# Kernel optimization log

Hardware: AMD Instinct MI355X
Metric: run time of the kernel (lower is better)

The kernel has to match this reference:

```python
import jax, jax.numpy as jnp
import numpy as np

N = 50000      # nodes
E = 800000     # edges (before self-loops)
IN = 128       # in_channels
H = 4          # heads
F = 32         # out_channels per head
NEG_SLOPE = 0.2  # GATConv default negative_slope


def setup_inputs() -> dict:
    key = jax.random.key(0)
    k1, k2, k3, k4, k5 = jax.random.split(key, 5)
    x = jax.random.normal(k1, (N, IN), dtype=jnp.float32)
    edge_index = jax.random.randint(k2, (2, E), 0, N, dtype=jnp.int32)
    W = jax.random.normal(k3, (IN, H * F), dtype=jnp.float32) * 0.05
    att_src = jax.random.normal(k4, (H, F), dtype=jnp.float32) * 0.05
    att_dst = jax.random.normal(k5, (H, F), dtype=jnp.float32) * 0.05
    bias = jnp.zeros((H * F,), dtype=jnp.float32)
    return {"x": x, "edge_index": edge_index, "W": W,
            "att_src": att_src, "att_dst": att_dst, "bias": bias}


def reference(x, edge_index, W, att_src, att_dst, bias):
    n = x.shape[0]
    # Linear projection, split into heads: [N, H, F]
    xp = (x @ W).reshape(n, H, F)
    # add_self_loops=True (GATConv default)
    loop = jnp.arange(n, dtype=edge_index.dtype)
    src = jnp.concatenate([edge_index[0], loop])  # [E+N]
    dst = jnp.concatenate([edge_index[1], loop])  # [E+N]
    # Per-node attention logits: [N, H]
    a_s = jnp.einsum('nhf,hf->nh', xp, att_src)
    a_d = jnp.einsum('nhf,hf->nh', xp, att_dst)
    # Edge logits + LeakyReLU: [E+N, H]
    e = jax.nn.leaky_relu(a_s[src] + a_d[dst], NEG_SLOPE)
    # Segment softmax over incoming edges of each dst node
    m = jax.ops.segment_max(e, dst, num_segments=n)  # every node has a self-loop
    e = jnp.exp(e - m[dst])
    denom = jax.ops.segment_sum(e, dst, num_segments=n)
    alpha = e / denom[dst]                     # [E+N, H]
    # Weighted aggregation of source features: [N, H, F]
    msg = alpha[:, :, None] * xp[src]
    out = jax.ops.segment_sum(msg, dst, num_segments=n)
    out = out.reshape(n, H * F) + bias         # concat heads + bias
    return jax.nn.relu(out)                    # wrapper activation (dropout = eval identity)
```

## Files before the change

### kernel.cpp

```cpp
#include <hip/hip_runtime.h>

#define HEADS 4
#define BSHIFT 8

typedef __attribute__((ext_vector_type(8))) short bf16x8;
typedef __attribute__((ext_vector_type(4))) float f32x4;

__device__ __forceinline__ unsigned short f2bf(float f) {
  unsigned u = __builtin_bit_cast(unsigned, f);
  u = (u + 0x7FFFu + ((u >> 16) & 1u)) >> 16;
  return (unsigned short)u;
}
__device__ __forceinline__ float bf2f(unsigned short s) {
  return __builtin_bit_cast(float, (unsigned)s << 16);
}
__device__ __forceinline__ float bf_lo(unsigned u) {
  return __builtin_bit_cast(float, u << 16);
}
__device__ __forceinline__ float bf_hi(unsigned u) {
  return __builtin_bit_cast(float, u & 0xFFFF0000u);
}

__global__ __launch_bounds__(256) void k_gemm(
    const float* __restrict__ x, const float* __restrict__ W,
    const float* __restrict__ att_src, const float* __restrict__ att_dst,
    unsigned* __restrict__ xpb, float* __restrict__ a_s, float* __restrict__ a_d,
    int* __restrict__ ghist, int n)
{
  __shared__ unsigned short xb[64 * 136];
  __shared__ unsigned short Wt[128 * 136];
  const int tid = threadIdx.x;
  const int row0 = blockIdx.x * 64;
  if (blockIdx.x == 0) ghist[tid] = 0;

  for (int u = tid; u < 2048; u += 256) {
    const int r = u >> 5, cq = u & 31;
    float4 v = make_float4(0.f, 0.f, 0.f, 0.f);
    if (row0 + r < n) v = ((const float4*)x)[(size_t)(row0 + r) * 32 + cq];
    unsigned short* p = &xb[r * 136 + cq * 4];
    p[0] = f2bf(v.x); p[1] = f2bf(v.y); p[2] = f2bf(v.z); p[3] = f2bf(v.w);
  }
  for (int u = tid; u < 4096; u += 256) {
    const int k = u >> 5, cq = u & 31;
    const float4 v = ((const float4*)W)[u];
    Wt[(4 * cq + 0) * 136 + k] = f2bf(v.x);
    Wt[(4 * cq + 1) * 136 + k] = f2bf(v.y);
    Wt[(4 * cq + 2) * 136 + k] = f2bf(v.z);
    Wt[(4 * cq + 3) * 136 + k] = f2bf(v.w);
  }
  __syncthreads();

  const int wv = tid >> 6;
  const int lane = tid & 63;
  const int r = lane & 15, g = lane >> 4;

  f32x4 acc[8];
#pragma unroll
  for (int t = 0; t < 8; ++t) acc[t] = (f32x4){0.f, 0.f, 0.f, 0.f};

  bf16x8 afr[4];
#pragma unroll
  for (int kc = 0; kc < 4; ++kc)
    afr[kc] = *(const bf16x8*)&xb[(16 * wv + r) * 136 + kc * 32 + g * 8];

#pragma unroll
  for (int kc = 0; kc < 4; ++kc) {
#pragma unroll
    for (int t = 0; t < 8; ++t) {
      const bf16x8 bfr = *(const bf16x8*)&Wt[(16 * t + r) * 136 + kc * 32 + g * 8];
      acc[t] = __builtin_amdgcn_mfma_f32_16x16x32_bf16(afr[kc], bfr, acc[t], 0, 0, 0);
    }
  }
  __syncthreads();

  unsigned short* obuf = Wt;
#pragma unroll
  for (int t = 0; t < 8; ++t) {
#pragma unroll
    for (int j = 0; j < 4; ++j)
      obuf[(16 * wv + 4 * g + j) * 132 + 16 * t + r] = f2bf(acc[t][j]);
  }
  __syncthreads();

  {
    const int row = tid >> 2, h = tid & 3;
    float ps = 0.f, pd = 0.f;
    const unsigned short* orow = &obuf[row * 132 + 32 * h];
#pragma unroll 8
    for (int j = 0; j < 32; ++j) {
      const float v = bf2f(orow[j]);
      ps += v * att_src[32 * h + j];
      pd += v * att_dst[32 * h + j];
    }
    if (row0 + row < n) {
      a_s[(row0 + row) * HEADS + h] = ps;
      a_d[(row0 + row) * HEADS + h] = pd;
    }
  }
  for (int u = tid; u < 2048; u += 256) {
    const int row = u >> 5, q = u & 31;
    if (row0 + row < n)
      ((uint2*)xpb)[(size_t)(row0 + row) * 32 + q] = *(const uint2*)&obuf[row * 132 + q * 4];
  }
}

__global__ __launch_bounds__(256) void k_hist(
    const int* __restrict__ dst, int* __restrict__ ghist, int E)
{
  __shared__ int h[256];
  const int t = threadIdx.x;
  h[t] = 0;
  __syncthreads();
  int i = blockIdx.x * 1024 + t;
#pragma unroll
  for (int k = 0; k < 4; ++k, i += 256)
    if (i < E) atomicAdd(&h[dst[i] >> BSHIFT], 1);
  __syncthreads();
  if (h[t]) atomicAdd(&ghist[t], h[t]);
}

__global__ __launch_bounds__(256) void k_bscan(
    const int* __restrict__ ghist, int* __restrict__ gstart, int* __restrict__ gcur)
{
  __shared__ int wsum[4];
  const int t = threadIdx.x, lane = t & 63, w = t >> 6;
  const int v = ghist[t];
  int s = v;
#pragma unroll
  for (int o = 1; o < 64; o <<= 1) { int u = __shfl_up(s, o); if (lane >= o) s += u; }
  if (lane == 63) wsum[w] = s;
  __syncthreads();
  int add = 0;
  for (int k = 0; k < w; ++k) add += wsum[k];
  const int excl = add + s - v;
  gstart[t] = excl;
  gcur[t] = excl;
  if (t == 255) gstart[256] = excl + v;
}

__global__ __launch_bounds__(256) void k_part(
    const int* __restrict__ src, const int* __restrict__ dst,
    int* __restrict__ gcur, unsigned* __restrict__ pbuf, int E)
{
  __shared__ unsigned sortbuf[4096];
  __shared__ int hist[256], lstart[256], lcur[256], wbase[256];
  __shared__ int wsum[4];
  const int t = threadIdx.x;
  const int e0 = blockIdx.x * 4096;
  const int cnt = min(4096, E - e0);
  hist[t] = 0;
  __syncthreads();
  for (int i = t; i < cnt; i += 256)
    atomicAdd(&hist[dst[e0 + i] >> BSHIFT], 1);
  __syncthreads();
  const int lane = t & 63, w = t >> 6;
  const int v = hist[t];
  int s = v;
#pragma unroll
  for (int o = 1; o < 64; o <<= 1) { int u = __shfl_up(s, o); if (lane >= o) s += u; }
  if (lane == 63) wsum[w] = s;
  __syncthreads();
  int add = 0;
  for (int k = 0; k < w; ++k) add += wsum[k];
  const int ls = add + s - v;
  lstart[t] = ls;
  lcur[t] = ls;
  wbase[t] = (v > 0) ? atomicAdd(&gcur[t], v) : 0;
  __syncthreads();
  for (int i = t; i < cnt; i += 256) {
    const int d = dst[e0 + i], sE = src[e0 + i];
    const int r = atomicAdd(&lcur[d >> BSHIFT], 1);
    sortbuf[r] = ((unsigned)d << 16) | (unsigned)sE;
  }
  __syncthreads();
  for (int i = t; i < cnt; i += 256) {
    const unsigned p = sortbuf[i];
    const int b = (int)(p >> (16 + BSHIFT));
    pbuf[wbase[b] + (i - lstart[b])] = p;
  }
}

__global__ __launch_bounds__(256) void k_fill2(
    const unsigned* __restrict__ pbuf, const int* __restrict__ gstart,
    int* __restrict__ offs, int* __restrict__ eidx, int n, int E)
{
  __shared__ int cnt[256], base[256];
  __shared__ int wsum[4];
  const int b = blockIdx.x, t = threadIdx.x;
  const int node0 = b << BSHIFT;
  const int ebeg = gstart[b], eend = gstart[b + 1];
  cnt[t] = 0;
  __syncthreads();
  for (int i = ebeg + t; i < eend; i += 256)
    atomicAdd(&cnt[(pbuf[i] >> 16) & 255], 1);
  __syncthreads();
  const int lane = t & 63, w = t >> 6;
  const int v = cnt[t];
  int s = v;
#pragma unroll
  for (int o = 1; o < 64; o <<= 1) { int u = __shfl_up(s, o); if (lane >= o) s += u; }
  if (lane == 63) wsum[w] = s;
  __syncthreads();
  int add = 0;
  for (int k = 0; k < w; ++k) add += wsum[k];
  base[t] = ebeg + add + s - v;
  if (node0 + t < n) offs[node0 + t] = base[t];
  __syncthreads();
  for (int i = ebeg + t; i < eend; i += 256) {
    const unsigned p = pbuf[i];
    const int pos = atomicAdd(&base[(p >> 16) & 255], 1);
    eidx[pos] = (int)(p & 0xFFFFu);
  }
  if (b == 0 && t == 0) offs[n] = E;
}

__global__ __launch_bounds__(256) void k_aggr(
    const unsigned* __restrict__ xpb, const float* __restrict__ a_s,
    const float* __restrict__ a_d, const int* __restrict__ offs,
    const int* __restrict__ eidx, const float* __restrict__ bias,
    float* __restrict__ out, int n)
{
  const int wid = (blockIdx.x * blockDim.x + threadIdx.x) >> 6;
  const int lane = threadIdx.x & 63;
  if (wid >= n) return;
  const int h = lane >> 4;

  const float adh = a_d[wid * HEADS + h];

  float l = a_s[wid * HEADS + h] + adh;
  l = l > 0.f ? l : 0.2f * l;
  const float pself = __expf(l);
  float den = pself;
  const unsigned uself = xpb[(size_t)wid * 64 + lane];
  float accx = pself * bf_lo(uself), accy = pself * bf_hi(uself);

  const int beg = offs[wid], end = offs[wid + 1];
  int e = beg;
  int nb = (end - beg) >> 2;

#define LOADB(s0, s1, s2, s3, u0, u1, u2, u3, b0, b1, b2, b3)            \
  {                                                                      \
    s0 = eidx[e]; s1 = eidx[e + 1]; s2 = eidx[e + 2]; s3 = eidx[e + 3];  \
    u0 = xpb[(size_t)s0 * 64 + lane]; b0 = a_s[s0 * HEADS + h];          \
    u1 = xpb[(size_t)s1 * 64 + lane]; b1 = a_s[s1 * HEADS + h];          \
    u2 = xpb[(size_t)s2 * 64 + lane]; b2 = a_s[s2 * HEADS + h];          \
    u3 = xpb[(size_t)s3 * 64 + lane]; b3 = a_s[s3 * HEADS + h];          \
    e += 4;                                                              \
  }
#define CONSUME(u0, u1, u2, u3, b0, b1, b2, b3)                          \
  {                                                                      \
    float l0 = b0 + adh; l0 = l0 > 0.f ? l0 : 0.2f * l0;                 \
    float l1 = b1 + adh; l1 = l1 > 0.f ? l1 : 0.2f * l1;                 \
    float l2 = b2 + adh; l2 = l2 > 0.f ? l2 : 0.2f * l2;                 \
    float l3 = b3 + adh; l3 = l3 > 0.f ? l3 : 0.2f * l3;                 \
    const float p0 = __expf(l0), p1 = __expf(l1);                        \
    const float p2 = __expf(l2), p3 = __expf(l3);                        \
    den += p0 + p1 + p2 + p3;                                            \
    accx += p0 * bf_lo(u0) + p1 * bf_lo(u1) + p2 * bf_lo(u2) + p3 * bf_lo(u3); \
    accy += p0 * bf_hi(u0) + p1 * bf_hi(u1) + p2 * bf_hi(u2) + p3 * bf_hi(u3); \
  }

  if (nb > 0) {
    int sa0, sa1, sa2, sa3, sb0, sb1, sb2, sb3;
    unsigned ua0, ua1, ua2, ua3, ub0, ub1, ub2, ub3;
    float ba0, ba1, ba2, ba3, bb0, bb1, bb2, bb3;
    LOADB(sa0, sa1, sa2, sa3, ua0, ua1, ua2, ua3, ba0, ba1, ba2, ba3);
    --nb;
    while (nb >= 2) {
      LOADB(sb0, sb1, sb2, sb3, ub0, ub1, ub2, ub3, bb0, bb1, bb2, bb3);
      CONSUME(ua0, ua1, ua2, ua3, ba0, ba1, ba2, ba3);
      LOADB(sa0, sa1, sa2, sa3, ua0, ua1, ua2, ua3, ba0, ba1, ba2, ba3);
      CONSUME(ub0, ub1, ub2, ub3, bb0, bb1, bb2, bb3);
      nb -= 2;
    }
    if (nb == 1) {
      LOADB(sb0, sb1, sb2, sb3, ub0, ub1, ub2, ub3, bb0, bb1, bb2, bb3);
      CONSUME(ua0, ua1, ua2, ua3, ba0, ba1, ba2, ba3);
      CONSUME(ub0, ub1, ub2, ub3, bb0, bb1, bb2, bb3);
    } else {
      CONSUME(ua0, ua1, ua2, ua3, ba0, ba1, ba2, ba3);
    }
  }
  for (; e < end; ++e) {
    const int s = eidx[e];
    const unsigned u = xpb[(size_t)s * 64 + lane];
    float lv = a_s[s * HEADS + h] + adh;
    lv = lv > 0.f ? lv : 0.2f * lv;
    const float p = __expf(lv);
    den += p;
    accx += p * bf_lo(u);
    accy += p * bf_hi(u);
  }
#undef LOADB
#undef CONSUME

  const float2 b2 = ((const float2*)bias)[lane];
  const float inv = 1.f / den;
  float ox = accx * inv + b2.x;
  float oy = accy * inv + b2.y;
  float2 o = make_float2(ox > 0.f ? ox : 0.f, oy > 0.f ? oy : 0.f);
  ((float2*)out)[(size_t)wid * 64 + lane] = o;
}

extern "C" void kernel_launch(void* const* d_in, const int* in_sizes, int n_in,
                              void* d_out, int out_size, void* d_ws, size_t ws_size,
                              hipStream_t stream) {
  const float* x       = (const float*)d_in[0];
  const int*   ei      = (const int*)d_in[1];
  const float* W       = (const float*)d_in[2];
  const float* att_src = (const float*)d_in[3];
  const float* att_dst = (const float*)d_in[4];
  const float* bias    = (const float*)d_in[5];
  float* out = (float*)d_out;
  const int n = in_sizes[0] / 128;
  const int E = in_sizes[1] / 2;
  const int* srce = ei;
  const int* dste = ei + E;

  char* ws = (char*)d_ws;
  size_t o = 0;
  unsigned* xpb = (unsigned*)(ws + o); o += (size_t)n * 128 * 2;
  o = (o + 255) & ~(size_t)255;
  float* a_s = (float*)(ws + o); o += (size_t)n * HEADS * 4;
  float* a_d = (float*)(ws + o); o += (size_t)n * HEADS * 4;
  int* ghist  = (int*)(ws + o);  o += 256 * 4;
  int* gstart = (int*)(ws + o);  o += 260 * 4;
  int* gcur   = (int*)(ws + o);  o += 256 * 4;
  int* offs   = (int*)(ws + o);  o += (size_t)(n + 4) * 4;
  int* eidx   = (int*)(ws + o);  o += (size_t)E * 4;
  unsigned* pbuf = (unsigned*)(ws + o); o += (size_t)E * 4;

  const int NB = (n + 255) >> BSHIFT;
  k_gemm<<<(n + 63) / 64, 256, 0, stream>>>(x, W, att_src, att_dst, xpb, a_s, a_d, ghist, n);
  k_hist<<<(E + 1023) / 1024, 256, 0, stream>>>(dste, ghist, E);
  k_bscan<<<1, 256, 0, stream>>>(ghist, gstart, gcur);
  k_part<<<(E + 4095) / 4096, 256, 0, stream>>>(srce, dste, gcur, pbuf, E);
  k_fill2<<<NB, 256, 0, stream>>>(pbuf, gstart, offs, eidx, n, E);
  k_aggr<<<(n + 3) / 4, 256, 0, stream>>>(xpb, a_s, a_d, offs, eidx, bias, out, n);
}
```

Measured before the change: 121.4 us.

## Precompute per-edge attention exponentials in CSR fill and pre-transpose W to bf16

The per-edge LeakyReLU and exp are moved out of the aggregation kernel into the CSR fill kernel, which writes a float4 of four per-head exponentials per edge in sorted order. The aggregation then reads those values instead of gathering a_s per source and computing exp once per lane. Separately, a small kernel converts and transposes W to bf16 once, so each GEMM block does vectorized copies instead of strided scalar conversions. This adds a 16-byte-per-edge buffer written and read back, plus an extra launch, in exchange for less repeated math and fewer scattered loads.

```diff
diff --git a/kernel.cpp b/kernel.cpp
--- a/kernel.cpp
+++ b/kernel.cpp
@@ -21,8 +21,16 @@
   return __builtin_bit_cast(float, u & 0xFFFF0000u);
 }
 
+__global__ __launch_bounds__(256) void k_wprep(
+    const float* __restrict__ W, unsigned short* __restrict__ Wtb)
+{
+  const int i = blockIdx.x * 256 + threadIdx.x;
+  const int c = i >> 7, k = i & 127;
+  Wtb[i] = f2bf(W[k * 128 + c]);
+}
+
 __global__ __launch_bounds__(256) void k_gemm(
-    const float* __restrict__ x, const float* __restrict__ W,
+    const float* __restrict__ x, const unsigned short* __restrict__ Wtb,
     const float* __restrict__ att_src, const float* __restrict__ att_dst,
     unsigned* __restrict__ xpb, float* __restrict__ a_s, float* __restrict__ a_d,
     int* __restrict__ ghist, int n)
@@ -40,13 +48,9 @@
     unsigned short* p = &xb[r * 136 + cq * 4];
     p[0] = f2bf(v.x); p[1] = f2bf(v.y); p[2] = f2bf(v.z); p[3] = f2bf(v.w);
   }
-  for (int u = tid; u < 4096; u += 256) {
-    const int k = u >> 5, cq = u & 31;
-    const float4 v = ((const float4*)W)[u];
-    Wt[(4 * cq + 0) * 136 + k] = f2bf(v.x);
-    Wt[(4 * cq + 1) * 136 + k] = f2bf(v.y);
-    Wt[(4 * cq + 2) * 136 + k] = f2bf(v.z);
-    Wt[(4 * cq + 3) * 136 + k] = f2bf(v.w);
+  for (int u = tid; u < 2048; u += 256) {
+    const int c = u >> 4, q = u & 15;
+    *(uint4*)&Wt[c * 136 + q * 8] = ((const uint4*)Wtb)[u];
   }
   __syncthreads();
 
@@ -182,14 +186,18 @@
 
 __global__ __launch_bounds__(256) void k_fill2(
     const unsigned* __restrict__ pbuf, const int* __restrict__ gstart,
-    int* __restrict__ offs, int* __restrict__ eidx, int n, int E)
+    const float* __restrict__ a_s, const float* __restrict__ a_d,
+    int* __restrict__ offs, int* __restrict__ eidx, float4* __restrict__ pflt,
+    int n, int E)
 {
   __shared__ int cnt[256], base[256];
+  __shared__ float4 adl[256];
   __shared__ int wsum[4];
   const int b = blockIdx.x, t = threadIdx.x;
   const int node0 = b << BSHIFT;
   const int ebeg = gstart[b], eend = gstart[b + 1];
   cnt[t] = 0;
+  if (node0 + t < n) adl[t] = ((const float4*)a_d)[node0 + t];
   __syncthreads();
   for (int i = ebeg + t; i < eend; i += 256)
     atomicAdd(&cnt[(pbuf[i] >> 16) & 255], 1);
@@ -208,8 +216,19 @@
   __syncthreads();
   for (int i = ebeg + t; i < eend; i += 256) {
     const unsigned p = pbuf[i];
-    const int pos = atomicAdd(&base[(p >> 16) & 255], 1);
-    eidx[pos] = (int)(p & 0xFFFFu);
+    const int dl = (p >> 16) & 255;
+    const int sn = (int)(p & 0xFFFFu);
+    const int pos = atomicAdd(&base[dl], 1);
+    eidx[pos] = sn;
+    const float4 as = ((const float4*)a_s)[sn];
+    const float4 ad = adl[dl];
+    float4 pv;
+    float l;
+    l = as.x + ad.x; l = fmaxf(l, 0.2f * l); pv.x = __expf(l);
+    l = as.y + ad.y; l = fmaxf(l, 0.2f * l); pv.y = __expf(l);
+    l = as.z + ad.z; l = fmaxf(l, 0.2f * l); pv.z = __expf(l);
+    l = as.w + ad.w; l = fmaxf(l, 0.2f * l); pv.w = __expf(l);
+    pflt[pos] = pv;
   }
   if (b == 0 && t == 0) offs[n] = E;
 }
@@ -217,18 +236,16 @@
 __global__ __launch_bounds__(256) void k_aggr(
     const unsigned* __restrict__ xpb, const float* __restrict__ a_s,
     const float* __restrict__ a_d, const int* __restrict__ offs,
-    const int* __restrict__ eidx, const float* __restrict__ bias,
-    float* __restrict__ out, int n)
+    const int* __restrict__ eidx, const float* __restrict__ pflt,
+    const float* __restrict__ bias, float* __restrict__ out, int n)
 {
   const int wid = (blockIdx.x * blockDim.x + threadIdx.x) >> 6;
   const int lane = threadIdx.x & 63;
   if (wid >= n) return;
   const int h = lane >> 4;
 
-  const float adh = a_d[wid * HEADS + h];
-
-  float l = a_s[wid * HEADS + h] + adh;
-  l = l > 0.f ? l : 0.2f * l;
+  float l = a_s[wid * HEADS + h] + a_d[wid * HEADS + h];
+  l = fmaxf(l, 0.2f * l);
   const float pself = __expf(l);
   float den = pself;
   const unsigned uself = xpb[(size_t)wid * 64 + lane];
@@ -238,23 +255,17 @@
   int e = beg;
   int nb = (end - beg) >> 2;
 
-#define LOADB(s0, s1, s2, s3, u0, u1, u2, u3, b0, b1, b2, b3)            \
+#define LOADB(s0, s1, s2, s3, u0, u1, u2, u3, p0, p1, p2, p3)            \
   {                                                                      \
     s0 = eidx[e]; s1 = eidx[e + 1]; s2 = eidx[e + 2]; s3 = eidx[e + 3];  \
-    u0 = xpb[(size_t)s0 * 64 + lane]; b0 = a_s[s0 * HEADS + h];          \
-    u1 = xpb[(size_t)s1 * 64 + lane]; b1 = a_s[s1 * HEADS + h];          \
-    u2 = xpb[(size_t)s2 * 64 + lane]; b2 = a_s[s2 * HEADS + h];          \
-    u3 = xpb[(size_t)s3 * 64 + lane]; b3 = a_s[s3 * HEADS + h];          \
+    p0 = pflt[(size_t)e * 4 + h];       u0 = xpb[(size_t)s0 * 64 + lane];\
+    p1 = pflt[(size_t)(e + 1) * 4 + h]; u1 = xpb[(size_t)s1 * 64 + lane];\
+    p2 = pflt[(size_t)(e + 2) * 4 + h]; u2 = xpb[(size_t)s2 * 64 + lane];\
+    p3 = pflt[(size_t)(e + 3) * 4 + h]; u3 = xpb[(size_t)s3 * 64 + lane];\
     e += 4;                                                              \
   }
-#define CONSUME(u0, u1, u2, u3, b0, b1, b2, b3)                          \
+#define CONSUME(u0, u1, u2, u3, p0, p1, p2, p3)                          \
   {                                                                      \
-    float l0 = b0 + adh; l0 = l0 > 0.f ? l0 : 0.2f * l0;                 \
-    float l1 = b1 + adh; l1 = l1 > 0.f ? l1 : 0.2f * l1;                 \
-    float l2 = b2 + adh; l2 = l2 > 0.f ? l2 : 0.2f * l2;                 \
-    float l3 = b3 + adh; l3 = l3 > 0.f ? l3 : 0.2f * l3;                 \
-    const float p0 = __expf(l0), p1 = __expf(l1);                        \
-    const float p2 = __expf(l2), p3 = __expf(l3);                        \
     den += p0 + p1 + p2 + p3;                                            \
     accx += p0 * bf_lo(u0) + p1 * bf_lo(u1) + p2 * bf_lo(u2) + p3 * bf_lo(u3); \
     accy += p0 * bf_hi(u0) + p1 * bf_hi(u1) + p2 * bf_hi(u2) + p3 * bf_hi(u3); \
@@ -263,30 +274,28 @@
   if (nb > 0) {
     int sa0, sa1, sa2, sa3, sb0, sb1, sb2, sb3;
     unsigned ua0, ua1, ua2, ua3, ub0, ub1, ub2, ub3;
-    float ba0, ba1, ba2, ba3, bb0, bb1, bb2, bb3;
-    LOADB(sa0, sa1, sa2, sa3, ua0, ua1, ua2, ua3, ba0, ba1, ba2, ba3);
+    float pa0, pa1, pa2, pa3, pb0, pb1, pb2, pb3;
+    LOADB(sa0, sa1, sa2, sa3, ua0, ua1, ua2, ua3, pa0, pa1, pa2, pa3);
     --nb;
     while (nb >= 2) {
-      LOADB(sb0, sb1, sb2, sb3, ub0, ub1, ub2, ub3, bb0, bb1, bb2, bb3);
-      CONSUME(ua0, ua1, ua2, ua3, ba0, ba1, ba2, ba3);
-      LOADB(sa0, sa1, sa2, sa3, ua0, ua1, ua2, ua3, ba0, ba1, ba2, ba3);
-      CONSUME(ub0, ub1, ub2, ub3, bb0, bb1, bb2, bb3);
+      LOADB(sb0, sb1, sb2, sb3, ub0, ub1, ub2, ub3, pb0, pb1, pb2, pb3);
+      CONSUME(ua0, ua1, ua2, ua3, pa0, pa1, pa2, pa3);
+      LOADB(sa0, sa1, sa2, sa3, ua0, ua1, ua2, ua3, pa0, pa1, pa2, pa3);
+      CONSUME(ub0, ub1, ub2, ub3, pb0, pb1, pb2, pb3);
       nb -= 2;
     }
     if (nb == 1) {
-      LOADB(sb0, sb1, sb2, sb3, ub0, ub1, ub2, ub3, bb0, bb1, bb2, bb3);
-      CONSUME(ua0, ua1, ua2, ua3, ba0, ba1, ba2, ba3);
-      CONSUME(ub0, ub1, ub2, ub3, bb0, bb1, bb2, bb3);
+      LOADB(sb0, sb1, sb2, sb3, ub0, ub1, ub2, ub3, pb0, pb1, pb2, pb3);
+      CONSUME(ua0, ua1, ua2, ua3, pa0, pa1, pa2, pa3);
+      CONSUME(ub0, ub1, ub2, ub3, pb0, pb1, pb2, pb3);
     } else {
-      CONSUME(ua0, ua1, ua2, ua3, ba0, ba1, ba2, ba3);
+      CONSUME(ua0, ua1, ua2, ua3, pa0, pa1, pa2, pa3);
     }
   }
   for (; e < end; ++e) {
     const int s = eidx[e];
     const unsigned u = xpb[(size_t)s * 64 + lane];
-    float lv = a_s[s * HEADS + h] + adh;
-    lv = lv > 0.f ? lv : 0.2f * lv;
-    const float p = __expf(lv);
+    const float p = pflt[(size_t)e * 4 + h];
     den += p;
     accx += p * bf_lo(u);
     accy += p * bf_hi(u);
@@ -323,18 +332,22 @@
   o = (o + 255) & ~(size_t)255;
   float* a_s = (float*)(ws + o); o += (size_t)n * HEADS * 4;
   float* a_d = (float*)(ws + o); o += (size_t)n * HEADS * 4;
+  unsigned short* Wtb = (unsigned short*)(ws + o); o += 128 * 128 * 2;
   int* ghist  = (int*)(ws + o);  o += 256 * 4;
   int* gstart = (int*)(ws + o);  o += 260 * 4;
   int* gcur   = (int*)(ws + o);  o += 256 * 4;
   int* offs   = (int*)(ws + o);  o += (size_t)(n + 4) * 4;
   int* eidx   = (int*)(ws + o);  o += (size_t)E * 4;
   unsigned* pbuf = (unsigned*)(ws + o); o += (size_t)E * 4;
+  o = (o + 15) & ~(size_t)15;
+  float4* pflt = (float4*)(ws + o); o += (size_t)E * 16;
 
   const int NB = (n + 255) >> BSHIFT;
-  k_gemm<<<(n + 63) / 64, 256, 0, stream>>>(x, W, att_src, att_dst, xpb, a_s, a_d, ghist, n);
+  k_wprep<<<64, 256, 0, stream>>>(W, Wtb);
+  k_gemm<<<(n + 63) / 64, 256, 0, stream>>>(x, Wtb, att_src, att_dst, xpb, a_s, a_d, ghist, n);
   k_hist<<<(E + 1023) / 1024, 256, 0, stream>>>(dste, ghist, E);
   k_bscan<<<1, 256, 0, stream>>>(ghist, gstart, gcur);
   k_part<<<(E + 4095) / 4096, 256, 0, stream>>>(srce, dste, gcur, pbuf, E);
-  k_fill2<<<NB, 256, 0, stream>>>(pbuf, gstart, offs, eidx, n, E);
-  k_aggr<<<(n + 3) / 4, 256, 0, stream>>>(xpb, a_s, a_d, offs, eidx, bias, out, n);
-}
+  k_fill2<<<NB, 256, 0, stream>>>(pbuf, gstart, a_s, a_d, offs, eidx, pflt, n, E);
+  k_aggr<<<(n + 3) / 4, 256, 0, stream>>>(xpb, a_s, a_d, offs, eidx, (const float*)pflt, bias, out, n);
+}
```

Result: slower. 125.1 us (+3.0%).

## Fuse GEMM, histogram and bucket scan into one launch with pre-transposed bf16 W

Applied to the files above, without the earlier changes.

Moves the W transpose and bf16 conversion into a small prep kernel so each GEMM block does one vectorized copy instead of a strided scatter into shared memory. The destination histogram and the bucket scan are merged into the GEMM launch as extra blocks, and the last histogram block, found through an atomic done counter, runs the scan. This drops two kernel launches and lets the histogram overlap the GEMM, at the cost of an extra small launch and a threadfence and atomic handshake. LeakyReLU is also rewritten as fmaxf in the aggregation kernel.

```diff
diff --git a/kernel.cpp b/kernel.cpp
--- a/kernel.cpp
+++ b/kernel.cpp
@@ -21,17 +21,65 @@
   return __builtin_bit_cast(float, u & 0xFFFF0000u);
 }
 
-__global__ __launch_bounds__(256) void k_gemm(
-    const float* __restrict__ x, const float* __restrict__ W,
+__global__ __launch_bounds__(256) void k_wprep(
+    const float* __restrict__ W, unsigned short* __restrict__ Wtb,
+    int* __restrict__ ghist, int* __restrict__ done)
+{
+  const int i = blockIdx.x * 256 + threadIdx.x;
+  const int c = i >> 7, k = i & 127;
+  Wtb[i] = f2bf(W[k * 128 + c]);
+  if (blockIdx.x == 0) {
+    ghist[threadIdx.x] = 0;
+    if (threadIdx.x == 0) *done = 0;
+  }
+}
+
+__global__ __launch_bounds__(256) void k_mega(
+    const float* __restrict__ x, const unsigned short* __restrict__ Wtb,
     const float* __restrict__ att_src, const float* __restrict__ att_dst,
     unsigned* __restrict__ xpb, float* __restrict__ a_s, float* __restrict__ a_d,
-    int* __restrict__ ghist, int n)
+    const int* __restrict__ dste, int* __restrict__ ghist, int* __restrict__ gstart,
+    int* __restrict__ gcur, int* __restrict__ done,
+    int n, int E, int GB, int NHB)
 {
   __shared__ unsigned short xb[64 * 136];
   __shared__ unsigned short Wt[128 * 136];
   const int tid = threadIdx.x;
+
+  if (blockIdx.x >= GB) {
+    int* h = (int*)xb;
+    h[tid] = 0;
+    __syncthreads();
+    int i = (blockIdx.x - GB) * 4096 + tid;
+#pragma unroll
+    for (int k = 0; k < 16; ++k, i += 256)
+      if (i < E) atomicAdd(&h[dste[i] >> BSHIFT], 1);
+    __syncthreads();
+    if (h[tid]) atomicAdd(&ghist[tid], h[tid]);
+    __threadfence();
+    __shared__ int lastFlag;
+    if (tid == 0) lastFlag = (atomicAdd(done, 1) == NHB - 1) ? 1 : 0;
+    __syncthreads();
+    if (lastFlag) {
+      __shared__ int wsum[4];
+      const int lane = tid & 63, w = tid >> 6;
+      const int v = atomicAdd(&ghist[tid], 0);
+      int s = v;
+#pragma unroll
+      for (int o = 1; o < 64; o <<= 1) { int u = __shfl_up(s, o); if (lane >= o) s += u; }
+      if (lane == 63) wsum[w] = s;
+      __syncthreads();
+      int add = 0;
+      for (int k = 0; k < w; ++k) add += wsum[k];
+      const int excl = add + s - v;
+      gstart[tid] = excl;
+      gcur[tid] = excl;
+      if (tid == 255) gstart[256] = excl + v;
+    }
+    return;
+  }
+
   const int row0 = blockIdx.x * 64;
-  if (blockIdx.x == 0) ghist[tid] = 0;
 
   for (int u = tid; u < 2048; u += 256) {
     const int r = u >> 5, cq = u & 31;
@@ -40,13 +88,9 @@
     unsigned short* p = &xb[r * 136 + cq * 4];
     p[0] = f2bf(v.x); p[1] = f2bf(v.y); p[2] = f2bf(v.z); p[3] = f2bf(v.w);
   }
-  for (int u = tid; u < 4096; u += 256) {
-    const int k = u >> 5, cq = u & 31;
-    const float4 v = ((const float4*)W)[u];
-    Wt[(4 * cq + 0) * 136 + k] = f2bf(v.x);
-    Wt[(4 * cq + 1) * 136 + k] = f2bf(v.y);
-    Wt[(4 * cq + 2) * 136 + k] = f2bf(v.z);
-    Wt[(4 * cq + 3) * 136 + k] = f2bf(v.w);
+  for (int u = tid; u < 2048; u += 256) {
+    const int c = u >> 4, q = u & 15;
+    *(uint4*)&Wt[c * 136 + q * 8] = ((const uint4*)Wtb)[u];
   }
   __syncthreads();
 
@@ -104,40 +148,6 @@
   }
 }
 
-__global__ __launch_bounds__(256) void k_hist(
-    const int* __restrict__ dst, int* __restrict__ ghist, int E)
-{
-  __shared__ int h[256];
-  const int t = threadIdx.x;
-  h[t] = 0;
-  __syncthreads();
-  int i = blockIdx.x * 1024 + t;
-#pragma unroll
-  for (int k = 0; k < 4; ++k, i += 256)
-    if (i < E) atomicAdd(&h[dst[i] >> BSHIFT], 1);
-  __syncthreads();
-  if (h[t]) atomicAdd(&ghist[t], h[t]);
-}
-
-__global__ __launch_bounds__(256) void k_bscan(
-    const int* __restrict__ ghist, int* __restrict__ gstart, int* __restrict__ gcur)
-{
-  __shared__ int wsum[4];
-  const int t = threadIdx.x, lane = t & 63, w = t >> 6;
-  const int v = ghist[t];
-  int s = v;
-#pragma unroll
-  for (int o = 1; o < 64; o <<= 1) { int u = __shfl_up(s, o); if (lane >= o) s += u; }
-  if (lane == 63) wsum[w] = s;
-  __syncthreads();
-  int add = 0;
-  for (int k = 0; k < w; ++k) add += wsum[k];
-  const int excl = add + s - v;
-  gstart[t] = excl;
-  gcur[t] = excl;
-  if (t == 255) gstart[256] = excl + v;
-}
-
 __global__ __launch_bounds__(256) void k_part(
     const int* __restrict__ src, const int* __restrict__ dst,
     int* __restrict__ gcur, unsigned* __restrict__ pbuf, int E)
@@ -228,7 +238,7 @@
   const float adh = a_d[wid * HEADS + h];
 
   float l = a_s[wid * HEADS + h] + adh;
-  l = l > 0.f ? l : 0.2f * l;
+  l = fmaxf(l, 0.2f * l);
   const float pself = __expf(l);
   float den = pself;
   const unsigned uself = xpb[(size_t)wid * 64 + lane];
@@ -249,10 +259,10 @@
   }
 #define CONSUME(u0, u1, u2, u3, b0, b1, b2, b3)                          \
   {                                                                      \
-    float l0 = b0 + adh; l0 = l0 > 0.f ? l0 : 0.2f * l0;                 \
-    float l1 = b1 + adh; l1 = l1 > 0.f ? l1 : 0.2f * l1;                 \
-    float l2 = b2 + adh; l2 = l2 > 0.f ? l2 : 0.2f * l2;                 \
-    float l3 = b3 + adh; l3 = l3 > 0.f ? l3 : 0.2f * l3;                 \
+    float l0 = b0 + adh; l0 = fmaxf(l0, 0.2f * l0);                      \
+    float l1 = b1 + adh; l1 = fmaxf(l1, 0.2f * l1);                      \
+    float l2 = b2 + adh; l2 = fmaxf(l2, 0.2f * l2);                      \
+    float l3 = b3 + adh; l3 = fmaxf(l3, 0.2f * l3);                      \
     const float p0 = __expf(l0), p1 = __expf(l1);                        \
     const float p2 = __expf(l2), p3 = __expf(l3);                        \
     den += p0 + p1 + p2 + p3;                                            \
@@ -285,7 +295,7 @@
     const int s = eidx[e];
     const unsigned u = xpb[(size_t)s * 64 + lane];
     float lv = a_s[s * HEADS + h] + adh;
-    lv = lv > 0.f ? lv : 0.2f * lv;
+    lv = fmaxf(lv, 0.2f * lv);
     const float p = __expf(lv);
     den += p;
     accx += p * bf_lo(u);
@@ -323,17 +333,21 @@
   o = (o + 255) & ~(size_t)255;
   float* a_s = (float*)(ws + o); o += (size_t)n * HEADS * 4;
   float* a_d = (float*)(ws + o); o += (size_t)n * HEADS * 4;
+  unsigned short* Wtb = (unsigned short*)(ws + o); o += 128 * 128 * 2;
   int* ghist  = (int*)(ws + o);  o += 256 * 4;
   int* gstart = (int*)(ws + o);  o += 260 * 4;
   int* gcur   = (int*)(ws + o);  o += 256 * 4;
+  int* done   = (int*)(ws + o);  o += 4 * 4;
   int* offs   = (int*)(ws + o);  o += (size_t)(n + 4) * 4;
   int* eidx   = (int*)(ws + o);  o += (size_t)E * 4;
   unsigned* pbuf = (unsigned*)(ws + o); o += (size_t)E * 4;
 
-  const int NB = (n + 255) >> BSHIFT;
-  k_gemm<<<(n + 63) / 64, 256, 0, stream>>>(x, W, att_src, att_dst, xpb, a_s, a_d, ghist, n);
-  k_hist<<<(E + 1023) / 1024, 256, 0, stream>>>(dste, ghist, E);
-  k_bscan<<<1, 256, 0, stream>>>(ghist, gstart, gcur);
+  const int GB  = (n + 63) / 64;
+  const int NHB = (E + 4095) / 4096;
+  const int NB  = (n + 255) >> BSHIFT;
+  k_wprep<<<64, 256, 0, stream>>>(W, Wtb, ghist, done);
+  k_mega<<<GB + NHB, 256, 0, stream>>>(x, Wtb, att_src, att_dst, xpb, a_s, a_d,
+                                       dste, ghist, gstart, gcur, done, n, E, GB, NHB);
   k_part<<<(E + 4095) / 4096, 256, 0, stream>>>(srce, dste, gcur, pbuf, E);
   k_fill2<<<NB, 256, 0, stream>>>(pbuf, gstart, offs, eidx, n, E);
   k_aggr<<<(n + 3) / 4, 256, 0, stream>>>(xpb, a_s, a_d, offs, eidx, bias, out, n);
```

New measurement: 111.9 us. -7.9%, faster.
